# Kernel optimization log

Measured on AMD Instinct MI355X. Metric: run time of the kernel, lower is better.

Reference implementation:

```python
import jax, jax.numpy as jnp
import numpy as np

B, GH, GW = 8, 32, 32
S = GH * GW            # 1024
HIDDEN = 512
D = 64                 # head_dim
NUM_HOPS = 2
EPS = 1e-6


def setup_inputs() -> dict:
    key = jax.random.key(0)
    ks = jax.random.split(key, 8)

    def init(k, shape, std):
        return (jax.random.normal(k, shape) * std).astype(jnp.float32)

    x = jax.random.normal(ks[0], (B, S, HIDDEN), dtype=jnp.float32)
    Wq = init(ks[1], (D, HIDDEN), HIDDEN ** -0.5)
    Wk = init(ks[2], (D, HIDDEN), HIDDEN ** -0.5)
    Wv = init(ks[3], (D, HIDDEN), HIDDEN ** -0.5)
    bias_table = init(ks[4], (2 * GH - 1, 2 * GW - 1), 0.02)
    fusion_w = jnp.ones((NUM_HOPS, 3), dtype=jnp.float32)
    fusion_b = jnp.zeros((NUM_HOPS,), dtype=jnp.float32)
    hop_W = init(ks[5], (NUM_HOPS, D, D), D ** -0.5)
    gate_W = init(ks[6], (NUM_HOPS, HIDDEN), HIDDEN ** -0.5)
    gate_b = jnp.zeros((NUM_HOPS,), dtype=jnp.float32)
    out_W = init(ks[7], (HIDDEN, D), D ** -0.5)
    temperature = jnp.ones((1,), dtype=jnp.float32)

    # relative position index [S, S] (buffer, constant)
    coords = np.stack(np.meshgrid(np.arange(GH), np.arange(GW), indexing='ij')).reshape(2, -1)
    rel = coords[:, :, None] - coords[:, None, :]
    rel[0] += GH - 1
    rel[1] += GW - 1
    rel_idx = jnp.asarray(rel[0] * (2 * GW - 1) + rel[1], dtype=jnp.int32)

    return dict(x=x, Wq=Wq, Wk=Wk, Wv=Wv, bias_table=bias_table,
                fusion_w=fusion_w, fusion_b=fusion_b, hop_W=hop_W,
                gate_W=gate_W, gate_b=gate_b, out_W=out_W,
                temperature=temperature, rel_idx=rel_idx)


def _rotate_half(u):
    d = u.shape[-1] // 2
    return jnp.concatenate([-u[..., d:], u[..., :d]], axis=-1)


def _prob_log(p):
    p = jnp.clip(p, EPS, 1.0 - EPS)
    return jnp.log(p / (1.0 - p + EPS))


def _mat_exp(M, h):
    R = M
    for _ in range(h - 1):
        R = jnp.matmul(R, M)
    return R


def _row_norm(M):
    return M / (jnp.sum(M, axis=-1, keepdims=True) + EPS)


def reference(x, Wq, Wk, Wv, bias_table, fusion_w, fusion_b, hop_W,
              gate_W, gate_b, out_W, temperature, rel_idx):
    b, s, hdim = x.shape
    d = Wq.shape[0]
    n_hops = hop_W.shape[0]
    scale = jnp.sqrt(jnp.float32(d))

    Q = jnp.einsum('bsh,dh->bsd', x, Wq)
    K = jnp.einsum('bsh,dh->bsd', x, Wk)
    V = jnp.einsum('bsh,dh->bsd', x, Wv)

    # RoPE (cached cos/sin are deterministic functions of S, D)
    inv_freq = 1.0 / (10000.0 ** (jnp.arange(0, d, 2, dtype=jnp.float32) / d))
    t = jnp.arange(s, dtype=jnp.float32)
    emb = jnp.concatenate([jnp.outer(t, inv_freq)] * 2, axis=-1)  # [S, D]
    cos, sin = jnp.cos(emb), jnp.sin(emb)
    Q = Q * cos + _rotate_half(Q) * sin
    K = K * cos + _rotate_half(K) * sin

    pb = bias_table.reshape(-1)[rel_idx]  # [S, S]
    scores = (jnp.einsum('bsd,btd->bst', Q, K) / scale + pb[None])
    scores = scores / jnp.clip(temperature, 0.1, None)
    A = jax.nn.softmax(scores, axis=-1)  # [B, S, S]

    A_T = jnp.swapaxes(A, -1, -2)
    AAt = jnp.matmul(A, A_T)
    AtA = jnp.matmul(A_T, A)

    hop_outs = []
    for hop in range(n_hops):
        h = hop + 1
        A_seq = _row_norm(_mat_exp(A, h))
        A_co = _row_norm(_mat_exp(AAt, h))
        A_sp = _row_norm(_mat_exp(AtA, h))
        fused_logit = (fusion_b[hop]
                       + fusion_w[hop, 0] * _prob_log(A_seq)
                       + fusion_w[hop, 1] * _prob_log(A_co)
                       + fusion_w[hop, 2] * _prob_log(A_sp))
        fused = _row_norm(jax.nn.sigmoid(fused_logit))
        hop_v = jnp.einsum('bsd,ed->bse', V, hop_W[hop])
        hop_outs.append(jnp.matmul(fused, hop_v))  # [B, S, D]

    gate = jax.nn.softmax(jnp.einsum('bsh,gh->bsg', x, gate_W) + gate_b, axis=-1)
    combined = sum(hop_outs[i] * gate[..., i:i + 1] for i in range(n_hops))
    return jnp.einsum('bsd,hd->bsh', combined, out_W)
```

## Files before the change

### kernel.cpp

```cpp
#include <hip/hip_runtime.h>
#include <hip/hip_bf16.h>

#define BB 8
#define SS 1024
#define HH 512
#define DD 64

typedef unsigned short u16;
typedef short v8s __attribute__((ext_vector_type(8)));
typedef float v4f __attribute__((ext_vector_type(4)));

__device__ __forceinline__ float bf2f(u16 u) {
    union { unsigned int i; float f; } v; v.i = ((unsigned int)u) << 16; return v.f;
}
__device__ __forceinline__ u16 f2bf(float f) {
    union { float f; unsigned int i; } v; v.f = f;
    unsigned int u = v.i;
    unsigned int r = u + 0x7fffu + ((u >> 16) & 1u);
    return (u16)(r >> 16);
}

__device__ __forceinline__ void gload16(const u16* g, u16* l) {
    __builtin_amdgcn_global_load_lds(
        (const __attribute__((address_space(1))) void*)g,
        (__attribute__((address_space(3))) void*)l,
        16, 0, 0);
}


__device__ __forceinline__ void tile_1024(
    const u16* __restrict__ Xb, const u16* __restrict__ Yb,
    u16* __restrict__ Cd, int tm, int tn, u16* Xs, u16* Ys)
{
    int t = threadIdx.x, lane = t & 63, w = t >> 6;
    int wm = (w & 1) << 6, wn = (w >> 1) << 6;
    int fr = lane & 15, q = lane >> 4, m7 = fr & 7;
    int subrow = lane >> 3, cch = (lane & 7) ^ subrow;

    const u16* xg[4]; const u16* yg[4]; u16* xl[4]; u16* yl[4];
    #pragma unroll
    for (int i = 0; i < 4; i++) {
        int r = i * 32 + w * 8 + subrow;
        xg[i] = Xb + (long)(tm + r) * 1024 + cch * 8;
        yg[i] = Yb + (long)(tn + r) * 1024 + cch * 8;
        xl[i] = Xs + (i * 32 + w * 8) * 64;
        yl[i] = Ys + (i * 32 + w * 8) * 64;
    }

    v4f acc[4][4];
    #pragma unroll
    for (int i = 0; i < 4; i++)
        #pragma unroll
        for (int j = 0; j < 4; j++) {
            acc[i][j][0] = 0.f; acc[i][j][1] = 0.f; acc[i][j][2] = 0.f; acc[i][j][3] = 0.f;
        }

    for (int k0 = 0; k0 < 1024; k0 += 64) {
        __syncthreads();
        #pragma unroll
        for (int i = 0; i < 4; i++) { gload16(xg[i] + k0, xl[i]); gload16(yg[i] + k0, yl[i]); }
        __syncthreads();
        v8s af[2][4], bfr[2][4];
        #pragma unroll
        for (int h = 0; h < 2; h++) {
            int ca = (((h << 2) + q) ^ m7) << 3;
            #pragma unroll
            for (int s = 0; s < 4; s++) {
                af[h][s]  = *(const v8s*)(Xs + (wm + s * 16 + fr) * 64 + ca);
                bfr[h][s] = *(const v8s*)(Ys + (wn + s * 16 + fr) * 64 + ca);
            }
        }
        #pragma unroll
        for (int h = 0; h < 2; h++)
            #pragma unroll
            for (int i = 0; i < 4; i++)
                #pragma unroll
                for (int j = 0; j < 4; j++)
                    acc[i][j] = __builtin_amdgcn_mfma_f32_16x16x32_bf16(af[h][i], bfr[h][j], acc[i][j], 0, 0, 0);
    }
    #pragma unroll
    for (int i = 0; i < 4; i++) {
        int rowb = tm + wm + i * 16 + q * 4;
        #pragma unroll
        for (int j = 0; j < 4; j++) {
            int col = tn + wn + j * 16 + fr;
            #pragma unroll
            for (int r = 0; r < 4; r++)
                Cd[(long)(rowb + r) * 1024 + col] = f2bf(acc[i][j][r]);
        }
    }
}

__global__ __launch_bounds__(256) void gemm_link1(
    const u16* __restrict__ A, const u16* __restrict__ AT,
    u16* __restrict__ AAt, u16* __restrict__ AtA, u16* __restrict__ A2)
{
    __shared__ u16 Xs[128 * 64];
    __shared__ u16 Ys[128 * 64];
    const long SSq = (long)SS * SS;
    int b = blockIdx.x & 7;
    int job = blockIdx.x >> 3;
    const u16* Xb; const u16* Yb; u16* Cd;
    int ti, tj;
    if (job < 72) {
        int tt = job < 36 ? job : job - 36;
        ti = 0;
        while (tt >= 8 - ti) { tt -= 8 - ti; ti++; }
        tj = ti + tt;
        if (job < 36) { Xb = A  + b * SSq; Yb = Xb; Cd = AAt + b * SSq; }
        else          { Xb = AT + b * SSq; Yb = Xb; Cd = AtA + b * SSq; }
    } else {
        int jj = job - 72;
        ti = jj >> 3; tj = jj & 7;
        Xb = A + b * SSq; Yb = AT + b * SSq; Cd = A2 + b * SSq;
    }
    tile_1024(Xb, Yb, Cd, ti * 128, tj * 128, Xs, Ys);
}

__global__ __launch_bounds__(256) void gemm_link2(
    const u16* __restrict__ X0, const u16* __restrict__ X1,
    u16* __restrict__ C0, u16* __restrict__ C1)
{
    __shared__ u16 Xs[128 * 64];
    __shared__ u16 Ys[128 * 64];
    const long SSq = (long)SS * SS;
    int z = blockIdx.x & 15;
    int tt = blockIdx.x >> 4, ti = 0;
    while (tt >= 8 - ti) { tt -= 8 - ti; ti++; }
    int tj = ti + tt;
    const u16* Xb = (z < 8 ? X0 : X1) + (long)(z & 7) * SSq;
    u16* Cd = (z < 8 ? C0 : C1) + (long)(z & 7) * SSq;
    tile_1024(Xb, Xb, Cd, ti * 128, tj * 128, Xs, Ys);
}

__global__ __launch_bounds__(256) void gemm_nt(
    const u16* __restrict__ X, long sx,
    const u16* __restrict__ Y, long sy,
    void* __restrict__ Cv, long sc,
    int M, int N, int K, int cf32)
{
    __shared__ u16 Xs[128 * 64];
    __shared__ u16 Ys[128 * 64];
    const u16* Xb = X + (long)blockIdx.z * sx;
    const u16* Yb = Y + (long)blockIdx.z * sy;
    int tm = blockIdx.x * 128, tn = blockIdx.y * 128;
    int t = threadIdx.x, lane = t & 63, w = t >> 6;
    int wm = (w & 1) << 6, wn = (w >> 1) << 6;
    int fr = lane & 15, q = lane >> 4, m7 = fr & 7;
    int subrow = lane >> 3, cch = (lane & 7) ^ subrow;

    const u16* xg[4]; const u16* yg[4]; u16* xl[4]; u16* yl[4];
    #pragma unroll
    for (int i = 0; i < 4; i++) {
        int r = i * 32 + w * 8 + subrow;
        xg[i] = Xb + (long)(tm + r) * K + cch * 8;
        yg[i] = Yb + (long)(tn + r) * K + cch * 8;
        xl[i] = Xs + (i * 32 + w * 8) * 64;
        yl[i] = Ys + (i * 32 + w * 8) * 64;
    }

    v4f acc[4][4];
    #pragma unroll
    for (int i = 0; i < 4; i++)
        #pragma unroll
        for (int j = 0; j < 4; j++) {
            acc[i][j][0] = 0.f; acc[i][j][1] = 0.f; acc[i][j][2] = 0.f; acc[i][j][3] = 0.f;
        }

    for (int k0 = 0; k0 < K; k0 += 64) {
        __syncthreads();
        #pragma unroll
        for (int i = 0; i < 4; i++) { gload16(xg[i] + k0, xl[i]); gload16(yg[i] + k0, yl[i]); }
        __syncthreads();
        v8s af[2][4], bfr[2][4];
        #pragma unroll
        for (int h = 0; h < 2; h++) {
            int ca = (((h << 2) + q) ^ m7) << 3;
            #pragma unroll
            for (int s = 0; s < 4; s++) {
                af[h][s]  = *(const v8s*)(Xs + (wm + s * 16 + fr) * 64 + ca);
                bfr[h][s] = *(const v8s*)(Ys + (wn + s * 16 + fr) * 64 + ca);
            }
        }
        #pragma unroll
        for (int h = 0; h < 2; h++)
            #pragma unroll
            for (int i = 0; i < 4; i++)
                #pragma unroll
                for (int j = 0; j < 4; j++)
                    acc[i][j] = __builtin_amdgcn_mfma_f32_16x16x32_bf16(af[h][i], bfr[h][j], acc[i][j], 0, 0, 0);
    }
    long cb = (long)blockIdx.z * sc;
    #pragma unroll
    for (int i = 0; i < 4; i++) {
        int rowb = tm + wm + i * 16 + q * 4;
        #pragma unroll
        for (int j = 0; j < 4; j++) {
            int col = tn + wn + j * 16 + fr;
            #pragma unroll
            for (int r = 0; r < 4; r++) {
                long o = cb + (long)(rowb + r) * N + col;
                if (cf32) ((float*)Cv)[o] = acc[i][j][r];
                else      ((u16*)Cv)[o] = f2bf(acc[i][j][r]);
            }
        }
    }
}

__global__ __launch_bounds__(256) void k_mirror(u16* __restrict__ C0, u16* __restrict__ C1)
{
    __shared__ u16 tile[128 * 136];
    const long SSq = (long)SS * SS;
    int z = blockIdx.z;
    u16* C = (z < 8 ? C0 : C1) + (long)(z & 7) * SSq;
    int tt = blockIdx.x, ti = 0;
    while (tt >= 7 - ti) { tt -= 7 - ti; ti++; }
    int tj = ti + 1 + tt;
    int t = threadIdx.x;
    int r = t >> 1, ch = (t & 1) << 6;
    const u16* src = C + (long)(ti * 128 + r) * 1024 + tj * 128 + ch;
    #pragma unroll
    for (int p = 0; p < 8; p++) {
        uint4 v = *(const uint4*)(src + p * 8);
        *(uint4*)(&tile[r * 136 + ch + p * 8]) = v;
    }
    __syncthreads();
    u16* dst = C + (long)(tj * 128 + r) * 1024 + ti * 128 + ch;
    #pragma unroll
    for (int p = 0; p < 8; p++) {
        uint4 ov; u16* po = (u16*)&ov;
        #pragma unroll
        for (int e = 0; e < 8; e++) po[e] = tile[(ch + p * 8 + e) * 136 + r];
        *(uint4*)(dst + p * 8) = ov;
    }
}

__global__ __launch_bounds__(256) void gemm_hop(
    const u16* __restrict__ F0, const u16* __restrict__ F1,
    const u16* __restrict__ H, float* __restrict__ P)
{
    __shared__ u16 Fs[128 * 64];
    __shared__ u16 Hs[64 * 64];
    const long SSq = (long)SS * SS;
    int z = blockIdx.z;
    const u16* Fb = (z < 8 ? F0 : F1) + (long)(z & 7) * SSq;
    const u16* Hb = H + (long)z * 65536;
    int tm = blockIdx.x * 128;
    int kb = blockIdx.y * 512;
    int t = threadIdx.x, lane = t & 63, w = t >> 6;
    int fr = lane & 15, q = lane >> 4, m7 = fr & 7;
    int subrow = lane >> 3, cch = (lane & 7) ^ subrow;

    const u16* fg[4]; u16* fl[4]; const u16* hg[2]; u16* hl[2];
    #pragma unroll
    for (int i = 0; i < 4; i++) {
        int r = i * 32 + w * 8 + subrow;
        fg[i] = Fb + (long)(tm + r) * 1024 + cch * 8;
        fl[i] = Fs + (i * 32 + w * 8) * 64;
    }
    #pragma unroll
    for (int i = 0; i < 2; i++) {
        int r = i * 32 + w * 8 + subrow;
        hg[i] = Hb + (long)r * 1024 + cch * 8;
        hl[i] = Hs + (i * 32 + w * 8) * 64;
    }

    v4f acc[2][4];
    #pragma unroll
    for (int i = 0; i < 2; i++)
        #pragma unroll
        for (int j = 0; j < 4; j++) {
            acc[i][j][0] = 0.f; acc[i][j][1] = 0.f; acc[i][j][2] = 0.f; acc[i][j][3] = 0.f;
        }

    for (int k0 = kb; k0 < kb + 512; k0 += 64) {
        __syncthreads();
        #pragma unroll
        for (int i = 0; i < 4; i++) gload16(fg[i] + k0, fl[i]);
        #pragma unroll
        for (int i = 0; i < 2; i++) gload16(hg[i] + k0, hl[i]);
        __syncthreads();
        v8s af[2][2], bfr[2][4];
        #pragma unroll
        for (int h = 0; h < 2; h++) {
            int ca = (((h << 2) + q) ^ m7) << 3;
            #pragma unroll
            for (int s = 0; s < 2; s++)
                af[h][s] = *(const v8s*)(Fs + (w * 32 + s * 16 + fr) * 64 + ca);
            #pragma unroll
            for (int s = 0; s < 4; s++)
                bfr[h][s] = *(const v8s*)(Hs + (s * 16 + fr) * 64 + ca);
        }
        #pragma unroll
        for (int h = 0; h < 2; h++)
            #pragma unroll
            for (int i = 0; i < 2; i++)
                #pragma unroll
                for (int j = 0; j < 4; j++)
                    acc[i][j] = __builtin_amdgcn_mfma_f32_16x16x32_bf16(af[h][i], bfr[h][j], acc[i][j], 0, 0, 0);
    }
    float* Pd = P + (long)(blockIdx.y * 16 + z) * 65536;
    #pragma unroll
    for (int i = 0; i < 2; i++) {
        int rowb = tm + w * 32 + i * 16 + q * 4;
        #pragma unroll
        for (int j = 0; j < 4; j++) {
            int col = j * 16 + fr;
            #pragma unroll
            for (int r = 0; r < 4; r++)
                Pd[(long)(rowb + r) * 64 + col] = acc[i][j][r];
        }
    }
}

__global__ __launch_bounds__(256) void k_packx(const float* __restrict__ src,
                                               u16* __restrict__ dst)
{
    long i = (long)blockIdx.x * 256 + threadIdx.x;
    float4 v = ((const float4*)src)[i];
    ushort4 o;
    o.x = f2bf(v.x); o.y = f2bf(v.y); o.z = f2bf(v.z); o.w = f2bf(v.w);
    ((ushort4*)dst)[i] = o;
}

__global__ __launch_bounds__(256) void k_packw(
    const float* __restrict__ Wq, const float* __restrict__ Wk,
    const float* __restrict__ Wv, const float* __restrict__ gW,
    const float* __restrict__ hopW, const float* __restrict__ outW,
    u16* __restrict__ wpack, u16* __restrict__ hopWb, u16* __restrict__ outWb)
{
    int idx = blockIdx.x * 256 + threadIdx.x;
    if (idx < 131072) {
        int r = idx >> 9, c = idx & 511;
        float v = 0.f;
        if (r < 64)       v = Wq[r * 512 + c];
        else if (r < 128) v = Wk[(r - 64) * 512 + c];
        else if (r < 192) v = Wv[(r - 128) * 512 + c];
        else if (r < 194) v = gW[(r - 192) * 512 + c];
        wpack[idx] = f2bf(v);
    } else if (idx < 131072 + 8192) {
        int i = idx - 131072;
        hopWb[i] = f2bf(hopW[i]);
    } else if (idx < 131072 + 8192 + 32768) {
        int i = idx - 131072 - 8192;
        outWb[i] = f2bf(outW[i]);
    }
}

__global__ __launch_bounds__(256) void k_rope(
    const float* __restrict__ QKVG, const float* __restrict__ gateb,
    u16* __restrict__ Qb, u16* __restrict__ Kb, u16* __restrict__ Vb,
    float* __restrict__ gate)
{
    int t = threadIdx.x, l = t & 63, w = t >> 6;
    long row = (long)blockIdx.x * 4 + w;
    int spos = (int)(row & (SS - 1));
    const float* base = QKVG + row * 256;
    float q = base[l], k = base[64 + l], v = base[128 + l];
    float qp = __shfl_xor(q, 32), kp = __shfl_xor(k, 32);
    float sgn = (l < 32) ? -1.f : 1.f;
    int f = l & 31;
    float ang = (float)spos * exp2f(-(float)f * (13.287712379549449f / 32.0f));
    float cs = cosf(ang), sn = sinf(ang);
    Qb[row * 64 + l] = f2bf(q * cs + sgn * qp * sn);
    Kb[row * 64 + l] = f2bf(k * cs + sgn * kp * sn);
    Vb[row * 64 + l] = f2bf(v);
    if (l < 2) {
        float g0 = base[192] + gateb[0], g1 = base[193] + gateb[1];
        float m = fmaxf(g0, g1);
        float e0 = __expf(g0 - m), e1 = __expf(g1 - m);
        gate[row * 2 + l] = ((l == 0) ? e0 : e1) / (e0 + e1);
    }
}

__global__ __launch_bounds__(256) void k_softmax(
    const float* __restrict__ scores, const float* __restrict__ btab,
    const float* __restrict__ temp, u16* __restrict__ A)
{
    __shared__ float bt[63 * 63];
    int t = threadIdx.x;
    for (int i = t; i < 3969; i += 256) bt[i] = btab[i];
    __syncthreads();
    int lane = t & 63, w = t >> 6;
    long row = (long)blockIdx.x * 4 + w;
    int i = (int)(row & 1023);
    int ih = i >> 5, iw = i & 31;
    float inv_t = 1.0f / fmaxf(temp[0], 0.1f);
    const float* srow = scores + row * 1024;
    float sc[16];
    float m = -1e30f;
    #pragma unroll
    for (int c = 0; c < 16; c++) {
        int j = c * 64 + lane;
        int jh = j >> 5, jw = j & 31;
        float pb = bt[(ih - jh + 31) * 63 + (iw - jw + 31)];
        float s = (srow[j] * 0.125f + pb) * inv_t;
        sc[c] = s; m = fmaxf(m, s);
    }
    #pragma unroll
    for (int o = 1; o < 64; o <<= 1) m = fmaxf(m, __shfl_xor(m, o));
    float sum = 0.f;
    #pragma unroll
    for (int c = 0; c < 16; c++) { sc[c] = __expf(sc[c] - m); sum += sc[c]; }
    #pragma unroll
    for (int o = 1; o < 64; o <<= 1) sum += __shfl_xor(sum, o);
    float inv = 1.0f / sum;
    #pragma unroll
    for (int c = 0; c < 16; c++) A[row * 1024 + c * 64 + lane] = f2bf(sc[c] * inv);
}

__global__ __launch_bounds__(256) void k_transpose(
    const u16* __restrict__ src, u16* __restrict__ dst,
    int srs, int drs, long sbs, long dbs)
{
    __shared__ u16 tile[64 * 72];
    const u16* s = src + (long)blockIdx.z * sbs;
    u16* d = dst + (long)blockIdx.z * dbs;
    int i0 = blockIdx.x * 64, j0 = blockIdx.y * 64;
    int t = threadIdx.x;
    int r = t >> 2, c0 = (t & 3) << 4;
    #pragma unroll
    for (int p = 0; p < 2; p++) {
        int c = c0 + p * 8;
        uint4 v = *(const uint4*)(s + (long)(i0 + r) * srs + j0 + c);
        *(uint4*)(&tile[r * 72 + c]) = v;
    }
    __syncthreads();
    #pragma unroll
    for (int p = 0; p < 2; p++) {
        uint4 ov;
        u16* po = (u16*)&ov;
        #pragma unroll
        for (int e = 0; e < 8; e++) po[e] = tile[(c0 + p * 8 + e) * 72 + r];
        *(uint4*)(d + (long)(j0 + r) * drs + i0 + c0 + p * 8) = ov;
    }
}

__global__ __launch_bounds__(256) void k_fused(
    const u16* __restrict__ M1, const u16* __restrict__ M2,
    const u16* __restrict__ M3, const float* __restrict__ fw,
    const float* __restrict__ fbv, int hop, u16* __restrict__ F)
{
    int t = threadIdx.x, lane = t & 63, w = t >> 6;
    long row = (long)blockIdx.x * 4 + w;
    const u16* r1 = M1 + row * 1024;
    const u16* r2 = M2 + row * 1024;
    const u16* r3 = M3 + row * 1024;
    float m1[16], m2[16], m3[16];
    float s1 = 0.f, s2 = 0.f, s3 = 0.f;
    #pragma unroll
    for (int c = 0; c < 16; c++) {
        int j = c * 64 + lane;
        m1[c] = bf2f(r1[j]); m2[c] = bf2f(r2[j]); m3[c] = bf2f(r3[j]);
        s1 += m1[c]; s2 += m2[c]; s3 += m3[c];
    }
    #pragma unroll
    for (int o = 1; o < 64; o <<= 1) {
        s1 += __shfl_xor(s1, o); s2 += __shfl_xor(s2, o); s3 += __shfl_xor(s3, o);
    }
    float i1 = 1.f / (s1 + 1e-6f), i2 = 1.f / (s2 + 1e-6f), i3 = 1.f / (s3 + 1e-6f);
    float w0 = fw[hop * 3], w1 = fw[hop * 3 + 1], w2 = fw[hop * 3 + 2], b0 = fbv[hop];
    float sig[16];
    float ssum = 0.f;
    #pragma unroll
    for (int c = 0; c < 16; c++) {
        float p1 = fminf(fmaxf(m1[c] * i1, 1e-6f), 1.0f - 1e-6f);
        float p2 = fminf(fmaxf(m2[c] * i2, 1e-6f), 1.0f - 1e-6f);
        float p3 = fminf(fmaxf(m3[c] * i3, 1e-6f), 1.0f - 1e-6f);
        float l1 = __logf(p1 / (1.0f - p1 + 1e-6f));
        float l2 = __logf(p2 / (1.0f - p2 + 1e-6f));
        float l3 = __logf(p3 / (1.0f - p3 + 1e-6f));
        float lg = b0 + w0 * l1 + w1 * l2 + w2 * l3;
        float sg = 1.0f / (1.0f + __expf(-lg));
        sig[c] = sg; ssum += sg;
    }
    #pragma unroll
    for (int o = 1; o < 64; o <<= 1) ssum += __shfl_xor(ssum, o);
    float inv = 1.0f / (ssum + 1e-6f);
    #pragma unroll
    for (int c = 0; c < 16; c++) F[row * 1024 + c * 64 + lane] = f2bf(sig[c] * inv);
}

__global__ __launch_bounds__(256) void k_combine(
    const float* __restrict__ P, const float* __restrict__ gate,
    u16* __restrict__ comb)
{
    long idx = (long)blockIdx.x * 256 + threadIdx.x;
    long srow = idx >> 6;
    int b = (int)(srow >> 10);
    long o = (long)(srow & 1023) * 64 + (idx & 63);
    float h0 = P[(long)(b) * 65536 + o]        + P[(long)(16 + b) * 65536 + o];
    float h1 = P[(long)(8 + b) * 65536 + o]    + P[(long)(24 + b) * 65536 + o];
    float g0 = gate[srow * 2], g1 = gate[srow * 2 + 1];
    comb[idx] = f2bf(h0 * g0 + h1 * g1);
}

extern "C" void kernel_launch(void* const* d_in, const int* in_sizes, int n_in,
                              void* d_out, int out_size, void* d_ws, size_t ws_size,
                              hipStream_t stream) {
    const float* x    = (const float*)d_in[0];
    const float* Wq   = (const float*)d_in[1];
    const float* Wk   = (const float*)d_in[2];
    const float* Wv   = (const float*)d_in[3];
    const float* btab = (const float*)d_in[4];
    const float* fw   = (const float*)d_in[5];
    const float* fbv  = (const float*)d_in[6];
    const float* hopW = (const float*)d_in[7];
    const float* gW   = (const float*)d_in[8];
    const float* gb   = (const float*)d_in[9];
    const float* outW = (const float*)d_in[10];
    const float* temp = (const float*)d_in[11];
    float* out = (float*)d_out;

    char* wsb = (char*)d_ws;
    size_t off = 0;
    auto take = [&](size_t n) { char* p = wsb + off; off += (n + 255) & ~(size_t)255; return p; };
    u16* Qb      = (u16*)take(8192L * 64 * 2);
    u16* Kb      = (u16*)take(8192L * 64 * 2);
    u16* Vb      = (u16*)take(8192L * 64 * 2);
    float* gate  = (float*)take(8192L * 2 * 4);
    u16* wpack   = (u16*)take(256L * 512 * 2);
    u16* hopWb   = (u16*)take(2L * 64 * 64 * 2);
    u16* outWb   = (u16*)take(512L * 64 * 2);
    u16* hopvC   = (u16*)take(8192L * 128 * 2);
    u16* hopVT   = (u16*)take(2L * 8 * 64 * 1024 * 2);
    float* P     = (float*)take(2L * 2 * 8 * 1024 * 64 * 4);
    u16* comb    = (u16*)take(8192L * 64 * 2);
    float* scoresF = (float*)take(8L * 1024 * 1024 * 4);
    float* QKVG  = (float*)scoresF;
    u16* F0      = (u16*)scoresF;
    u16* F1      = (u16*)scoresF + 8L * 1024 * 1024;
    u16* A       = (u16*)take(8L * 1024 * 1024 * 2);
    u16* xb      = (u16*)A;
    u16* AT      = (u16*)take(8L * 1024 * 1024 * 2);
    u16* AAt     = (u16*)take(8L * 1024 * 1024 * 2);
    u16* AtA     = (u16*)take(8L * 1024 * 1024 * 2);
    u16* A2      = (u16*)take(8L * 1024 * 1024 * 2);
    u16* AAt2    = (u16*)take(8L * 1024 * 1024 * 2);
    u16* AtA2    = (u16*)take(8L * 1024 * 1024 * 2);
    (void)ws_size; (void)in_sizes; (void)n_in; (void)out_size;

    const long SD = (long)SS * DD;
    const long SSq = (long)SS * SS;

    k_packx<<<4096, 256, 0, stream>>>(x, xb);
    k_packw<<<672, 256, 0, stream>>>(Wq, Wk, Wv, gW, hopW, outW, wpack, hopWb, outWb);
    gemm_nt<<<dim3(64, 2, 1), 256, 0, stream>>>(xb, 0, wpack, 0, QKVG, 0, 8192, 256, 512, 1);
    k_rope<<<2048, 256, 0, stream>>>(QKVG, gb, Qb, Kb, Vb, gate);
    gemm_nt<<<dim3(64, 1, 1), 256, 0, stream>>>(Vb, 0, hopWb, 0, hopvC, 0, 8192, 128, 64, 0);
    k_transpose<<<dim3(16, 1, 8), 256, 0, stream>>>(hopvC, hopVT, 128, 1024, 1024L * 128, 65536L);
    k_transpose<<<dim3(16, 1, 8), 256, 0, stream>>>(hopvC + 64, hopVT + 8L * 65536, 128, 1024, 1024L * 128, 65536L);
    gemm_nt<<<dim3(8, 8, 8), 256, 0, stream>>>(Qb, SD, Kb, SD, scoresF, SSq, 1024, 1024, 64, 1);
    k_softmax<<<2048, 256, 0, stream>>>(scoresF, btab, temp, A);
    k_transpose<<<dim3(16, 16, 8), 256, 0, stream>>>(A, AT, 1024, 1024, SSq, SSq);
    gemm_link1<<<1088, 256, 0, stream>>>(A, AT, AAt, AtA, A2);
    k_mirror<<<dim3(28, 1, 16), 256, 0, stream>>>(AAt, AtA);
    k_fused<<<2048, 256, 0, stream>>>(A, AAt, AtA, fw, fbv, 0, F0);
    gemm_link2<<<576, 256, 0, stream>>>(AAt, AtA, AAt2, AtA2);
    k_mirror<<<dim3(28, 1, 16), 256, 0, stream>>>(AAt2, AtA2);
    k_fused<<<2048, 256, 0, stream>>>(A2, AAt2, AtA2, fw, fbv, 1, F1);
    gemm_hop<<<dim3(8, 2, 16), 256, 0, stream>>>(F0, F1, hopVT, P);
    k_combine<<<2048, 256, 0, stream>>>(P, gate, comb);
    gemm_nt<<<dim3(64, 4, 1), 256, 0, stream>>>(comb, 0, outWb, 0, out, 0, 8192, 512, 64, 1);
}
```

Before: 335.7 us.

## Co-schedule independent stages into shared launches to cut kernel count

```diff
diff --git a/kernel.cpp b/kernel.cpp
--- a/kernel.cpp
+++ b/kernel.cpp
@@ -89,6 +89,192 @@
                 Cd[(long)(rowb + r) * 1024 + col] = f2bf(acc[i][j][r]);
         }
     }
+}
+
+__device__ __forceinline__ void tile_k64(
+    const u16* __restrict__ Xrows, const u16* __restrict__ Yrows,
+    void* __restrict__ Cd, int crs, int cf32, u16* Xs, u16* Ys)
+{
+    int t = threadIdx.x, lane = t & 63, w = t >> 6;
+    int wm = (w & 1) << 6, wn = (w >> 1) << 6;
+    int fr = lane & 15, q = lane >> 4, m7 = fr & 7;
+    int subrow = lane >> 3, cch = (lane & 7) ^ subrow;
+
+    #pragma unroll
+    for (int i = 0; i < 4; i++) {
+        int r = i * 32 + w * 8 + subrow;
+        gload16(Xrows + (long)r * 64 + cch * 8, Xs + (i * 32 + w * 8) * 64);
+        gload16(Yrows + (long)r * 64 + cch * 8, Ys + (i * 32 + w * 8) * 64);
+    }
+    __syncthreads();
+
+    v4f acc[4][4];
+    #pragma unroll
+    for (int i = 0; i < 4; i++)
+        #pragma unroll
+        for (int j = 0; j < 4; j++) {
+            acc[i][j][0] = 0.f; acc[i][j][1] = 0.f; acc[i][j][2] = 0.f; acc[i][j][3] = 0.f;
+        }
+    v8s af[2][4], bfr[2][4];
+    #pragma unroll
+    for (int h = 0; h < 2; h++) {
+        int ca = (((h << 2) + q) ^ m7) << 3;
+        #pragma unroll
+        for (int s = 0; s < 4; s++) {
+            af[h][s]  = *(const v8s*)(Xs + (wm + s * 16 + fr) * 64 + ca);
+            bfr[h][s] = *(const v8s*)(Ys + (wn + s * 16 + fr) * 64 + ca);
+        }
+    }
+    #pragma unroll
+    for (int h = 0; h < 2; h++)
+        #pragma unroll
+        for (int i = 0; i < 4; i++)
+            #pragma unroll
+            for (int j = 0; j < 4; j++)
+                acc[i][j] = __builtin_amdgcn_mfma_f32_16x16x32_bf16(af[h][i], bfr[h][j], acc[i][j], 0, 0, 0);
+    #pragma unroll
+    for (int i = 0; i < 4; i++) {
+        int rowb = wm + i * 16 + q * 4;
+        #pragma unroll
+        for (int j = 0; j < 4; j++) {
+            int col = wn + j * 16 + fr;
+            #pragma unroll
+            for (int r = 0; r < 4; r++) {
+                long o = (long)(rowb + r) * crs + col;
+                if (cf32) ((float*)Cd)[o] = acc[i][j][r];
+                else      ((u16*)Cd)[o] = f2bf(acc[i][j][r]);
+            }
+        }
+    }
+}
+
+__device__ __forceinline__ void hop_tile(
+    const u16* __restrict__ Fb, const u16* __restrict__ Hb,
+    int y, int tmt, float* __restrict__ Pd, u16* Fs, u16* Hs)
+{
+    int tm = tmt * 128, kb = y * 256;
+    int t = threadIdx.x, lane = t & 63, w = t >> 6;
+    int fr = lane & 15, q = lane >> 4, m7 = fr & 7;
+    int subrow = lane >> 3, cch = (lane & 7) ^ subrow;
+
+    const u16* fg[4]; u16* fl[4]; const u16* hg[2]; u16* hl[2];
+    #pragma unroll
+    for (int i = 0; i < 4; i++) {
+        int r = i * 32 + w * 8 + subrow;
+        fg[i] = Fb + (long)(tm + r) * 1024 + cch * 8;
+        fl[i] = Fs + (i * 32 + w * 8) * 64;
+    }
+    #pragma unroll
+    for (int i = 0; i < 2; i++) {
+        int r = i * 32 + w * 8 + subrow;
+        hg[i] = Hb + (long)r * 1024 + cch * 8;
+        hl[i] = Hs + (i * 32 + w * 8) * 64;
+    }
+
+    v4f acc[2][4];
+    #pragma unroll
+    for (int i = 0; i < 2; i++)
+        #pragma unroll
+        for (int j = 0; j < 4; j++) {
+            acc[i][j][0] = 0.f; acc[i][j][1] = 0.f; acc[i][j][2] = 0.f; acc[i][j][3] = 0.f;
+        }
+
+    for (int k0 = kb; k0 < kb + 256; k0 += 64) {
+        __syncthreads();
+        #pragma unroll
+        for (int i = 0; i < 4; i++) gload16(fg[i] + k0, fl[i]);
+        #pragma unroll
+        for (int i = 0; i < 2; i++) gload16(hg[i] + k0, hl[i]);
+        __syncthreads();
+        v8s af[2][2], bfr[2][4];
+        #pragma unroll
+        for (int h = 0; h < 2; h++) {
+            int ca = (((h << 2) + q) ^ m7) << 3;
+            #pragma unroll
+            for (int s = 0; s < 2; s++)
+                af[h][s] = *(const v8s*)(Fs + (w * 32 + s * 16 + fr) * 64 + ca);
+            #pragma unroll
+            for (int s = 0; s < 4; s++)
+                bfr[h][s] = *(const v8s*)(Hs + (s * 16 + fr) * 64 + ca);
+        }
+        #pragma unroll
+        for (int h = 0; h < 2; h++)
+            #pragma unroll
+            for (int i = 0; i < 2; i++)
+                #pragma unroll
+                for (int j = 0; j < 4; j++)
+                    acc[i][j] = __builtin_amdgcn_mfma_f32_16x16x32_bf16(af[h][i], bfr[h][j], acc[i][j], 0, 0, 0);
+    }
+    #pragma unroll
+    for (int i = 0; i < 2; i++) {
+        int rowb = tm + w * 32 + i * 16 + q * 4;
+        #pragma unroll
+        for (int j = 0; j < 4; j++) {
+            int col = j * 16 + fr;
+            #pragma unroll
+            for (int r = 0; r < 4; r++)
+                Pd[(long)(rowb + r) * 64 + col] = acc[i][j][r];
+        }
+    }
+}
+
+__device__ __forceinline__ void mirror_tile(u16* __restrict__ C, int ti, int tj, u16* sm)
+{
+    int t = threadIdx.x;
+    int r = t >> 1, ch = (t & 1) << 6;
+    const u16* src = C + (long)(ti * 128 + r) * 1024 + tj * 128 + ch;
+    #pragma unroll
+    for (int p = 0; p < 8; p++) {
+        uint4 v = *(const uint4*)(src + p * 8);
+        *(uint4*)(&sm[r * 136 + ch + p * 8]) = v;
+    }
+    __syncthreads();
+    u16* dst = C + (long)(tj * 128 + r) * 1024 + ti * 128 + ch;
+    #pragma unroll
+    for (int p = 0; p < 8; p++) {
+        uint4 ov; u16* po = (u16*)&ov;
+        #pragma unroll
+        for (int e = 0; e < 8; e++) po[e] = sm[(ch + p * 8 + e) * 136 + r];
+        *(uint4*)(dst + p * 8) = ov;
+    }
+}
+
+__device__ __forceinline__ void fused_row(
+    const u16* __restrict__ r1, const u16* __restrict__ r2, const u16* __restrict__ r3,
+    float w0, float w1, float w2, float b0, u16* __restrict__ Frow, int lane)
+{
+    float m1[16], m2[16], m3[16];
+    float s1 = 0.f, s2 = 0.f, s3 = 0.f;
+    #pragma unroll
+    for (int c = 0; c < 16; c++) {
+        int j = c * 64 + lane;
+        m1[c] = bf2f(r1[j]); m2[c] = bf2f(r2[j]); m3[c] = bf2f(r3[j]);
+        s1 += m1[c]; s2 += m2[c]; s3 += m3[c];
+    }
+    #pragma unroll
+    for (int o = 1; o < 64; o <<= 1) {
+        s1 += __shfl_xor(s1, o); s2 += __shfl_xor(s2, o); s3 += __shfl_xor(s3, o);
+    }
+    float i1 = 1.f / (s1 + 1e-6f), i2 = 1.f / (s2 + 1e-6f), i3 = 1.f / (s3 + 1e-6f);
+    float sig[16];
+    float ssum = 0.f;
+    #pragma unroll
+    for (int c = 0; c < 16; c++) {
+        float p1 = fminf(fmaxf(m1[c] * i1, 1e-6f), 1.0f - 1e-6f);
+        float p2 = fminf(fmaxf(m2[c] * i2, 1e-6f), 1.0f - 1e-6f);
+        float p3 = fminf(fmaxf(m3[c] * i3, 1e-6f), 1.0f - 1e-6f);
+        float l1 = __logf(p1 / (1.0f - p1 + 1e-6f));
+        float l2 = __logf(p2 / (1.0f - p2 + 1e-6f));
+        float l3 = __logf(p3 / (1.0f - p3 + 1e-6f));
+        float lg = b0 + w0 * l1 + w1 * l2 + w2 * l3;
+        float sg = 1.0f / (1.0f + __expf(-lg));
+        sig[c] = sg; ssum += sg;
+    }
+    #pragma unroll
+    for (int o = 1; o < 64; o <<= 1) ssum += __shfl_xor(ssum, o);
+    float inv = 1.0f / (ssum + 1e-6f);
+    #pragma unroll
+    for (int c = 0; c < 16; c++) Frow[c * 64 + lane] = f2bf(sig[c] * inv);
 }
 
 __global__ __launch_bounds__(256) void gemm_link1(
@@ -117,20 +303,76 @@
     tile_1024(Xb, Yb, Cd, ti * 128, tj * 128, Xs, Ys);
 }
 
-__global__ __launch_bounds__(256) void gemm_link2(
-    const u16* __restrict__ X0, const u16* __restrict__ X1,
-    u16* __restrict__ C0, u16* __restrict__ C1)
+__global__ __launch_bounds__(256) void k_g2f0(
+    const u16* __restrict__ AAt, const u16* __restrict__ AtA,
+    u16* __restrict__ AAt2, u16* __restrict__ AtA2,
+    const u16* __restrict__ A, const float* __restrict__ fw,
+    const float* __restrict__ fbv, u16* __restrict__ F0)
 {
     __shared__ u16 Xs[128 * 64];
     __shared__ u16 Ys[128 * 64];
     const long SSq = (long)SS * SS;
-    int z = blockIdx.x & 15;
-    int tt = blockIdx.x >> 4, ti = 0;
-    while (tt >= 8 - ti) { tt -= 8 - ti; ti++; }
-    int tj = ti + tt;
-    const u16* Xb = (z < 8 ? X0 : X1) + (long)(z & 7) * SSq;
-    u16* Cd = (z < 8 ? C0 : C1) + (long)(z & 7) * SSq;
-    tile_1024(Xb, Xb, Cd, ti * 128, tj * 128, Xs, Ys);
+    int bx = blockIdx.x;
+    if (bx < 576) {
+        int z = bx & 15;
+        int tt = bx >> 4, ti = 0;
+        while (tt >= 8 - ti) { tt -= 8 - ti; ti++; }
+        int tj = ti + tt;
+        const u16* Xb = (z < 8 ? AAt : AtA) + (long)(z & 7) * SSq;
+        u16* Cd = (z < 8 ? AAt2 : AtA2) + (long)(z & 7) * SSq;
+        tile_1024(Xb, Xb, Cd, ti * 128, tj * 128, Xs, Ys);
+    } else {
+        int f = bx - 576;
+        int lane = threadIdx.x & 63, w = threadIdx.x >> 6;
+        float w0 = fw[0], w1 = fw[1], w2 = fw[2], b0 = fbv[0];
+        #pragma unroll
+        for (int r = 0; r < 4; r++) {
+            long row = (long)f * 16 + w * 4 + r;
+            fused_row(A + row * 1024, AAt + row * 1024, AtA + row * 1024,
+                      w0, w1, w2, b0, F0 + row * 1024, lane);
+        }
+    }
+}
+
+__global__ __launch_bounds__(256) void k_m2h0(
+    u16* __restrict__ AAt2, u16* __restrict__ AtA2,
+    const u16* __restrict__ F0, const u16* __restrict__ hopVT,
+    float* __restrict__ Pa, float* __restrict__ Pb)
+{
+    __shared__ __align__(16) u16 sm[128 * 136];
+    const long SSq = (long)SS * SS;
+    int bx = blockIdx.x;
+    if (bx < 448) {
+        int z = bx & 15;
+        int tt = bx >> 4, ti = 0;
+        while (tt >= 7 - ti) { tt -= 7 - ti; ti++; }
+        int tj = ti + 1 + tt;
+        u16* C = (z < 8 ? AAt2 : AtA2) + (long)(z & 7) * SSq;
+        mirror_tile(C, ti, tj, sm);
+    } else {
+        int j = bx - 448;
+        int y = j >> 6, rest = j & 63;
+        int tmt = rest >> 3, b = rest & 7;
+        float* Pd = (y < 2 ? Pa + (long)y * 16 * 65536 : Pb + (long)(y - 2) * 16 * 65536)
+                    + (long)b * 65536;
+        hop_tile(F0 + (long)b * SSq, hopVT + (long)b * 65536, y, tmt, Pd,
+                 sm, sm + 128 * 64);
+    }
+}
+
+__global__ __launch_bounds__(256) void gemm_hop1(
+    const u16* __restrict__ F1, const u16* __restrict__ hopVT,
+    float* __restrict__ Pa, float* __restrict__ Pb)
+{
+    __shared__ u16 Fs[128 * 64];
+    __shared__ u16 Hs[64 * 64];
+    const long SSq = (long)SS * SS;
+    int j = blockIdx.x;
+    int y = j >> 6, rest = j & 63;
+    int tmt = rest >> 3, b = rest & 7;
+    float* Pd = (y < 2 ? Pa + (long)y * 16 * 65536 : Pb + (long)(y - 2) * 16 * 65536)
+                + (long)(8 + b) * 65536;
+    hop_tile(F1 + (long)b * SSq, hopVT + (long)(8 + b) * 65536, y, tmt, Pd, Fs, Hs);
 }
 
 __global__ __launch_bounds__(256) void gemm_nt(
@@ -207,143 +449,149 @@
     }
 }
 
+__global__ __launch_bounds__(256) void k_qk_hopv(
+    const u16* __restrict__ Qb, const u16* __restrict__ Kb,
+    const u16* __restrict__ Vb, const u16* __restrict__ hopWb,
+    float* __restrict__ scores, u16* __restrict__ hopvC)
+{
+    __shared__ u16 Xs[128 * 64];
+    __shared__ u16 Ys[128 * 64];
+    const long SSq = (long)SS * SS;
+    const long SD = (long)SS * DD;
+    int bx = blockIdx.x;
+    if (bx < 512) {
+        int z = bx & 7;
+        int tt = bx >> 3;
+        int tm = (tt >> 3) * 128, tn = (tt & 7) * 128;
+        tile_k64(Qb + z * SD + (long)tm * 64, Kb + z * SD + (long)tn * 64,
+                 scores + z * SSq + (long)tm * 1024 + tn, 1024, 1, Xs, Ys);
+    } else {
+        int tm = (bx - 512) * 128;
+        tile_k64(Vb + (long)tm * 64, hopWb,
+                 hopvC + (long)tm * 128, 128, 0, Xs, Ys);
+    }
+}
+
+__global__ __launch_bounds__(256) void k_sm_hvt(
+    const float* __restrict__ scores, const float* __restrict__ btab,
+    const float* __restrict__ temp, u16* __restrict__ A,
+    const u16* __restrict__ hopvC, u16* __restrict__ hopVT)
+{
+    __shared__ __align__(16) float smf[3969];
+    int bx = blockIdx.x;
+    int t = threadIdx.x;
+    if (bx < 2048) {
+        for (int i = t; i < 3969; i += 256) smf[i] = btab[i];
+        __syncthreads();
+        int lane = t & 63, w = t >> 6;
+        long row = (long)bx * 4 + w;
+        int i = (int)(row & 1023);
+        int ih = i >> 5, iw = i & 31;
+        float inv_t = 1.0f / fmaxf(temp[0], 0.1f);
+        const float* srow = scores + row * 1024;
+        float sc[16];
+        float m = -1e30f;
+        #pragma unroll
+        for (int c = 0; c < 16; c++) {
+            int j = c * 64 + lane;
+            int jh = j >> 5, jw = j & 31;
+            float pb = smf[(ih - jh + 31) * 63 + (iw - jw + 31)];
+            float s = (srow[j] * 0.125f + pb) * inv_t;
+            sc[c] = s; m = fmaxf(m, s);
+        }
+        #pragma unroll
+        for (int o = 1; o < 64; o <<= 1) m = fmaxf(m, __shfl_xor(m, o));
+        float sum = 0.f;
+        #pragma unroll
+        for (int c = 0; c < 16; c++) { sc[c] = __expf(sc[c] - m); sum += sc[c]; }
+        #pragma unroll
+        for (int o = 1; o < 64; o <<= 1) sum += __shfl_xor(sum, o);
+        float inv = 1.0f / sum;
+        #pragma unroll
+        for (int c = 0; c < 16; c++) A[row * 1024 + c * 64 + lane] = f2bf(sc[c] * inv);
+    } else {
+        u16* tile = (u16*)smf;
+        int ex = bx - 2048;
+        int hop = ex >> 7, rem = ex & 127;
+        int z = rem & 7, i0 = (rem >> 3) * 64;
+        const u16* s = hopvC + (long)z * (1024 * 128) + hop * 64;
+        u16* d = hopVT + (long)(hop * 8 + z) * 65536;
+        int r = t >> 2, c0 = (t & 3) << 4;
+        #pragma unroll
+        for (int p = 0; p < 2; p++) {
+            int c = c0 + p * 8;
+            uint4 v = *(const uint4*)(s + (long)(i0 + r) * 128 + c);
+            *(uint4*)(&tile[r * 72 + c]) = v;
+        }
+        __syncthreads();
+        #pragma unroll
+        for (int p = 0; p < 2; p++) {
+            uint4 ov; u16* po = (u16*)&ov;
+            #pragma unroll
+            for (int e = 0; e < 8; e++) po[e] = tile[(c0 + p * 8 + e) * 72 + r];
+            *(uint4*)(d + (long)r * 1024 + i0 + c0 + p * 8) = ov;
+        }
+    }
+}
+
 __global__ __launch_bounds__(256) void k_mirror(u16* __restrict__ C0, u16* __restrict__ C1)
 {
-    __shared__ u16 tile[128 * 136];
+    __shared__ __align__(16) u16 sm[128 * 136];
     const long SSq = (long)SS * SS;
     int z = blockIdx.z;
     u16* C = (z < 8 ? C0 : C1) + (long)(z & 7) * SSq;
     int tt = blockIdx.x, ti = 0;
     while (tt >= 7 - ti) { tt -= 7 - ti; ti++; }
     int tj = ti + 1 + tt;
-    int t = threadIdx.x;
-    int r = t >> 1, ch = (t & 1) << 6;
-    const u16* src = C + (long)(ti * 128 + r) * 1024 + tj * 128 + ch;
-    #pragma unroll
-    for (int p = 0; p < 8; p++) {
-        uint4 v = *(const uint4*)(src + p * 8);
-        *(uint4*)(&tile[r * 136 + ch + p * 8]) = v;
-    }
-    __syncthreads();
-    u16* dst = C + (long)(tj * 128 + r) * 1024 + ti * 128 + ch;
-    #pragma unroll
-    for (int p = 0; p < 8; p++) {
-        uint4 ov; u16* po = (u16*)&ov;
-        #pragma unroll
-        for (int e = 0; e < 8; e++) po[e] = tile[(ch + p * 8 + e) * 136 + r];
-        *(uint4*)(dst + p * 8) = ov;
-    }
-}
-
-__global__ __launch_bounds__(256) void gemm_hop(
-    const u16* __restrict__ F0, const u16* __restrict__ F1,
-    const u16* __restrict__ H, float* __restrict__ P)
-{
-    __shared__ u16 Fs[128 * 64];
-    __shared__ u16 Hs[64 * 64];
-    const long SSq = (long)SS * SS;
-    int z = blockIdx.z;
-    const u16* Fb = (z < 8 ? F0 : F1) + (long)(z & 7) * SSq;
-    const u16* Hb = H + (long)z * 65536;
-    int tm = blockIdx.x * 128;
-    int kb = blockIdx.y * 512;
-    int t = threadIdx.x, lane = t & 63, w = t >> 6;
-    int fr = lane & 15, q = lane >> 4, m7 = fr & 7;
-    int subrow = lane >> 3, cch = (lane & 7) ^ subrow;
-
-    const u16* fg[4]; u16* fl[4]; const u16* hg[2]; u16* hl[2];
-    #pragma unroll
-    for (int i = 0; i < 4; i++) {
-        int r = i * 32 + w * 8 + subrow;
-        fg[i] = Fb + (long)(tm + r) * 1024 + cch * 8;
-        fl[i] = Fs + (i * 32 + w * 8) * 64;
-    }
-    #pragma unroll
-    for (int i = 0; i < 2; i++) {
-        int r = i * 32 + w * 8 + subrow;
-        hg[i] = Hb + (long)r * 1024 + cch * 8;
-        hl[i] = Hs + (i * 32 + w * 8) * 64;
-    }
-
-    v4f acc[2][4];
-    #pragma unroll
-    for (int i = 0; i < 2; i++)
-        #pragma unroll
-        for (int j = 0; j < 4; j++) {
-            acc[i][j][0] = 0.f; acc[i][j][1] = 0.f; acc[i][j][2] = 0.f; acc[i][j][3] = 0.f;
-        }
-
-    for (int k0 = kb; k0 < kb + 512; k0 += 64) {
-        __syncthreads();
-        #pragma unroll
-        for (int i = 0; i < 4; i++) gload16(fg[i] + k0, fl[i]);
-        #pragma unroll
-        for (int i = 0; i < 2; i++) gload16(hg[i] + k0, hl[i]);
-        __syncthreads();
-        v8s af[2][2], bfr[2][4];
-        #pragma unroll
-        for (int h = 0; h < 2; h++) {
-            int ca = (((h << 2) + q) ^ m7) << 3;
-            #pragma unroll
-            for (int s = 0; s < 2; s++)
-                af[h][s] = *(const v8s*)(Fs + (w * 32 + s * 16 + fr) * 64 + ca);
-            #pragma unroll
-            for (int s = 0; s < 4; s++)
-                bfr[h][s] = *(const v8s*)(Hs + (s * 16 + fr) * 64 + ca);
-        }
-        #pragma unroll
-        for (int h = 0; h < 2; h++)
-            #pragma unroll
-            for (int i = 0; i < 2; i++)
-                #pragma unroll
-                for (int j = 0; j < 4; j++)
-                    acc[i][j] = __builtin_amdgcn_mfma_f32_16x16x32_bf16(af[h][i], bfr[h][j], acc[i][j], 0, 0, 0);
-    }
-    float* Pd = P + (long)(blockIdx.y * 16 + z) * 65536;
-    #pragma unroll
-    for (int i = 0; i < 2; i++) {
-        int rowb = tm + w * 32 + i * 16 + q * 4;
-        #pragma unroll
-        for (int j = 0; j < 4; j++) {
-            int col = j * 16 + fr;
-            #pragma unroll
-            for (int r = 0; r < 4; r++)
-                Pd[(long)(rowb + r) * 64 + col] = acc[i][j][r];
-        }
-    }
-}
-
-__global__ __launch_bounds__(256) void k_packx(const float* __restrict__ src,
-                                               u16* __restrict__ dst)
-{
-    long i = (long)blockIdx.x * 256 + threadIdx.x;
-    float4 v = ((const float4*)src)[i];
-    ushort4 o;
-    o.x = f2bf(v.x); o.y = f2bf(v.y); o.z = f2bf(v.z); o.w = f2bf(v.w);
-    ((ushort4*)dst)[i] = o;
-}
-
-__global__ __launch_bounds__(256) void k_packw(
-    const float* __restrict__ Wq, const float* __restrict__ Wk,
-    const float* __restrict__ Wv, const float* __restrict__ gW,
-    const float* __restrict__ hopW, const float* __restrict__ outW,
+    mirror_tile(C, ti, tj, sm);
+}
+
+__global__ __launch_bounds__(256) void k_fused1(
+    const u16* __restrict__ A2, const u16* __restrict__ AAt2,
+    const u16* __restrict__ AtA2, const float* __restrict__ fw,
+    const float* __restrict__ fbv, u16* __restrict__ F1)
+{
+    int lane = threadIdx.x & 63, w = threadIdx.x >> 6;
+    float w0 = fw[3], w1 = fw[4], w2 = fw[5], b0 = fbv[1];
+    #pragma unroll
+    for (int r = 0; r < 4; r++) {
+        long row = (long)blockIdx.x * 16 + w * 4 + r;
+        fused_row(A2 + row * 1024, AAt2 + row * 1024, AtA2 + row * 1024,
+                  w0, w1, w2, b0, F1 + row * 1024, lane);
+    }
+}
+
+__global__ __launch_bounds__(256) void k_pack(
+    const float* __restrict__ x, const float* __restrict__ Wq,
+    const float* __restrict__ Wk, const float* __restrict__ Wv,
+    const float* __restrict__ gW, const float* __restrict__ hopW,
+    const float* __restrict__ outW, u16* __restrict__ xb,
     u16* __restrict__ wpack, u16* __restrict__ hopWb, u16* __restrict__ outWb)
 {
-    int idx = blockIdx.x * 256 + threadIdx.x;
-    if (idx < 131072) {
-        int r = idx >> 9, c = idx & 511;
-        float v = 0.f;
-        if (r < 64)       v = Wq[r * 512 + c];
-        else if (r < 128) v = Wk[(r - 64) * 512 + c];
-        else if (r < 192) v = Wv[(r - 128) * 512 + c];
-        else if (r < 194) v = gW[(r - 192) * 512 + c];
-        wpack[idx] = f2bf(v);
-    } else if (idx < 131072 + 8192) {
-        int i = idx - 131072;
-        hopWb[i] = f2bf(hopW[i]);
-    } else if (idx < 131072 + 8192 + 32768) {
-        int i = idx - 131072 - 8192;
-        outWb[i] = f2bf(outW[i]);
+    int bx = blockIdx.x;
+    if (bx < 4096) {
+        long i = (long)bx * 256 + threadIdx.x;
+        float4 v = ((const float4*)x)[i];
+        ushort4 o;
+        o.x = f2bf(v.x); o.y = f2bf(v.y); o.z = f2bf(v.z); o.w = f2bf(v.w);
+        ((ushort4*)xb)[i] = o;
+    } else {
+        int idx = (bx - 4096) * 256 + threadIdx.x;
+        if (idx < 131072) {
+            int r = idx >> 9, c = idx & 511;
+            float v = 0.f;
+            if (r < 64)       v = Wq[r * 512 + c];
+            else if (r < 128) v = Wk[(r - 64) * 512 + c];
+            else if (r < 192) v = Wv[(r - 128) * 512 + c];
+            else if (r < 194) v = gW[(r - 192) * 512 + c];
+            wpack[idx] = f2bf(v);
+        } else if (idx < 131072 + 8192) {
+            int i = idx - 131072;
+            hopWb[i] = f2bf(hopW[i]);
+        } else if (idx < 131072 + 8192 + 32768) {
+            int i = idx - 131072 - 8192;
+            outWb[i] = f2bf(outW[i]);
+        }
     }
 }
 
@@ -373,42 +621,6 @@
     }
 }
 
-__global__ __launch_bounds__(256) void k_softmax(
-    const float* __restrict__ scores, const float* __restrict__ btab,
-    const float* __restrict__ temp, u16* __restrict__ A)
-{
-    __shared__ float bt[63 * 63];
-    int t = threadIdx.x;
-    for (int i = t; i < 3969; i += 256) bt[i] = btab[i];
-    __syncthreads();
-    int lane = t & 63, w = t >> 6;
-    long row = (long)blockIdx.x * 4 + w;
-    int i = (int)(row & 1023);
-    int ih = i >> 5, iw = i & 31;
-    float inv_t = 1.0f / fmaxf(temp[0], 0.1f);
-    const float* srow = scores + row * 1024;
-    float sc[16];
-    float m = -1e30f;
-    #pragma unroll
-    for (int c = 0; c < 16; c++) {
-        int j = c * 64 + lane;
-        int jh = j >> 5, jw = j & 31;
-        float pb = bt[(ih - jh + 31) * 63 + (iw - jw + 31)];
-        float s = (srow[j] * 0.125f + pb) * inv_t;
-        sc[c] = s; m = fmaxf(m, s);
-    }
-    #pragma unroll
-    for (int o = 1; o < 64; o <<= 1) m = fmaxf(m, __shfl_xor(m, o));
-    float sum = 0.f;
-    #pragma unroll
-    for (int c = 0; c < 16; c++) { sc[c] = __expf(sc[c] - m); sum += sc[c]; }
-    #pragma unroll
-    for (int o = 1; o < 64; o <<= 1) sum += __shfl_xor(sum, o);
-    float inv = 1.0f / sum;
-    #pragma unroll
-    for (int c = 0; c < 16; c++) A[row * 1024 + c * 64 + lane] = f2bf(sc[c] * inv);
-}
-
 __global__ __launch_bounds__(256) void k_transpose(
     const u16* __restrict__ src, u16* __restrict__ dst,
     int srs, int drs, long sbs, long dbs)
@@ -436,61 +648,18 @@
     }
 }
 
-__global__ __launch_bounds__(256) void k_fused(
-    const u16* __restrict__ M1, const u16* __restrict__ M2,
-    const u16* __restrict__ M3, const float* __restrict__ fw,
-    const float* __restrict__ fbv, int hop, u16* __restrict__ F)
-{
-    int t = threadIdx.x, lane = t & 63, w = t >> 6;
-    long row = (long)blockIdx.x * 4 + w;
-    const u16* r1 = M1 + row * 1024;
-    const u16* r2 = M2 + row * 1024;
-    const u16* r3 = M3 + row * 1024;
-    float m1[16], m2[16], m3[16];
-    float s1 = 0.f, s2 = 0.f, s3 = 0.f;
-    #pragma unroll
-    for (int c = 0; c < 16; c++) {
-        int j = c * 64 + lane;
-        m1[c] = bf2f(r1[j]); m2[c] = bf2f(r2[j]); m3[c] = bf2f(r3[j]);
-        s1 += m1[c]; s2 += m2[c]; s3 += m3[c];
-    }
-    #pragma unroll
-    for (int o = 1; o < 64; o <<= 1) {
-        s1 += __shfl_xor(s1, o); s2 += __shfl_xor(s2, o); s3 += __shfl_xor(s3, o);
-    }
-    float i1 = 1.f / (s1 + 1e-6f), i2 = 1.f / (s2 + 1e-6f), i3 = 1.f / (s3 + 1e-6f);
-    float w0 = fw[hop * 3], w1 = fw[hop * 3 + 1], w2 = fw[hop * 3 + 2], b0 = fbv[hop];
-    float sig[16];
-    float ssum = 0.f;
-    #pragma unroll
-    for (int c = 0; c < 16; c++) {
-        float p1 = fminf(fmaxf(m1[c] * i1, 1e-6f), 1.0f - 1e-6f);
-        float p2 = fminf(fmaxf(m2[c] * i2, 1e-6f), 1.0f - 1e-6f);
-        float p3 = fminf(fmaxf(m3[c] * i3, 1e-6f), 1.0f - 1e-6f);
-        float l1 = __logf(p1 / (1.0f - p1 + 1e-6f));
-        float l2 = __logf(p2 / (1.0f - p2 + 1e-6f));
-        float l3 = __logf(p3 / (1.0f - p3 + 1e-6f));
-        float lg = b0 + w0 * l1 + w1 * l2 + w2 * l3;
-        float sg = 1.0f / (1.0f + __expf(-lg));
-        sig[c] = sg; ssum += sg;
-    }
-    #pragma unroll
-    for (int o = 1; o < 64; o <<= 1) ssum += __shfl_xor(ssum, o);
-    float inv = 1.0f / (ssum + 1e-6f);
-    #pragma unroll
-    for (int c = 0; c < 16; c++) F[row * 1024 + c * 64 + lane] = f2bf(sig[c] * inv);
-}
-
 __global__ __launch_bounds__(256) void k_combine(
-    const float* __restrict__ P, const float* __restrict__ gate,
-    u16* __restrict__ comb)
+    const float* __restrict__ Pa, const float* __restrict__ Pb,
+    const float* __restrict__ gate, u16* __restrict__ comb)
 {
     long idx = (long)blockIdx.x * 256 + threadIdx.x;
     long srow = idx >> 6;
     int b = (int)(srow >> 10);
     long o = (long)(srow & 1023) * 64 + (idx & 63);
-    float h0 = P[(long)(b) * 65536 + o]        + P[(long)(16 + b) * 65536 + o];
-    float h1 = P[(long)(8 + b) * 65536 + o]    + P[(long)(24 + b) * 65536 + o];
+    float h0 = Pa[(long)b * 65536 + o] + Pa[(long)(16 + b) * 65536 + o]
+             + Pb[(long)b * 65536 + o] + Pb[(long)(16 + b) * 65536 + o];
+    float h1 = Pa[(long)(8 + b) * 65536 + o] + Pa[(long)(24 + b) * 65536 + o]
+             + Pb[(long)(8 + b) * 65536 + o] + Pb[(long)(24 + b) * 65536 + o];
     float g0 = gate[srow * 2], g1 = gate[srow * 2 + 1];
     comb[idx] = f2bf(h0 * g0 + h1 * g1);
 }
@@ -524,7 +693,7 @@
     u16* outWb   = (u16*)take(512L * 64 * 2);
     u16* hopvC   = (u16*)take(8192L * 128 * 2);
     u16* hopVT   = (u16*)take(2L * 8 * 64 * 1024 * 2);
-    float* P     = (float*)take(2L * 2 * 8 * 1024 * 64 * 4);
+    float* Pa    = (float*)take(2L * 16 * 65536 * 4);
     u16* comb    = (u16*)take(8192L * 64 * 2);
     float* scoresF = (float*)take(8L * 1024 * 1024 * 4);
     float* QKVG  = (float*)scoresF;
@@ -533,6 +702,7 @@
     u16* A       = (u16*)take(8L * 1024 * 1024 * 2);
     u16* xb      = (u16*)A;
     u16* AT      = (u16*)take(8L * 1024 * 1024 * 2);
+    float* Pb    = (float*)AT;
     u16* AAt     = (u16*)take(8L * 1024 * 1024 * 2);
     u16* AtA     = (u16*)take(8L * 1024 * 1024 * 2);
     u16* A2      = (u16*)take(8L * 1024 * 1024 * 2);
@@ -540,26 +710,20 @@
     u16* AtA2    = (u16*)take(8L * 1024 * 1024 * 2);
     (void)ws_size; (void)in_sizes; (void)n_in; (void)out_size;
 
-    const long SD = (long)SS * DD;
     const long SSq = (long)SS * SS;
 
-    k_packx<<<4096, 256, 0, stream>>>(x, xb);
-    k_packw<<<672, 256, 0, stream>>>(Wq, Wk, Wv, gW, hopW, outW, wpack, hopWb, outWb);
+    k_pack<<<4768, 256, 0, stream>>>(x, Wq, Wk, Wv, gW, hopW, outW, xb, wpack, hopWb, outWb);
     gemm_nt<<<dim3(64, 2, 1), 256, 0, stream>>>(xb, 0, wpack, 0, QKVG, 0, 8192, 256, 512, 1);
     k_rope<<<2048, 256, 0, stream>>>(QKVG, gb, Qb, Kb, Vb, gate);
-    gemm_nt<<<dim3(64, 1, 1), 256, 0, stream>>>(Vb, 0, hopWb, 0, hopvC, 0, 8192, 128, 64, 0);
-    k_transpose<<<dim3(16, 1, 8), 256, 0, stream>>>(hopvC, hopVT, 128, 1024, 1024L * 128, 65536L);
-    k_transpose<<<dim3(16, 1, 8), 256, 0, stream>>>(hopvC + 64, hopVT + 8L * 65536, 128, 1024, 1024L * 128, 65536L);
-    gemm_nt<<<dim3(8, 8, 8), 256, 0, stream>>>(Qb, SD, Kb, SD, scoresF, SSq, 1024, 1024, 64, 1);
-    k_softmax<<<2048, 256, 0, stream>>>(scoresF, btab, temp, A);
+    k_qk_hopv<<<576, 256, 0, stream>>>(Qb, Kb, Vb, hopWb, scoresF, hopvC);
+    k_sm_hvt<<<2304, 256, 0, stream>>>(scoresF, btab, temp, A, hopvC, hopVT);
     k_transpose<<<dim3(16, 16, 8), 256, 0, stream>>>(A, AT, 1024, 1024, SSq, SSq);
     gemm_link1<<<1088, 256, 0, stream>>>(A, AT, AAt, AtA, A2);
     k_mirror<<<dim3(28, 1, 16), 256, 0, stream>>>(AAt, AtA);
-    k_fused<<<2048, 256, 0, stream>>>(A, AAt, AtA, fw, fbv, 0, F0);
-    gemm_link2<<<576, 256, 0, stream>>>(AAt, AtA, AAt2, AtA2);
-    k_mirror<<<dim3(28, 1, 16), 256, 0, stream>>>(AAt2, AtA2);
-    k_fused<<<2048, 256, 0, stream>>>(A2, AAt2, AtA2, fw, fbv, 1, F1);
-    gemm_hop<<<dim3(8, 2, 16), 256, 0, stream>>>(F0, F1, hopVT, P);
-    k_combine<<<2048, 256, 0, stream>>>(P, gate, comb);
+    k_g2f0<<<1088, 256, 0, stream>>>(AAt, AtA, AAt2, AtA2, A, fw, fbv, F0);
+    k_m2h0<<<704, 256, 0, stream>>>(AAt2, AtA2, F0, hopVT, Pa, Pb);
+    k_fused1<<<512, 256, 0, stream>>>(A2, AAt2, AtA2, fw, fbv, F1);
+    gemm_hop1<<<256, 256, 0, stream>>>(F1, hopVT, Pa, Pb);
+    k_combine<<<2048, 256, 0, stream>>>(Pa, Pb, gate, comb);
     gemm_nt<<<dim3(64, 4, 1), 256, 0, stream>>>(comb, 0, outWb, 0, out, 0, 8192, 512, 64, 1);
 }
```

Measured after the change: 321.9 us. 1.04x faster.
